# Kernel optimization log

Hardware: AMD Instinct MI355X
Metric: run time of the kernel (lower is better)

Reference implementation:

```python
import jax, jax.numpy as jnp
import numpy as np

N_NODES = 100_000
N_EDGES = 800_000
D_EDGE = 64
D_NODE = 64
D_GLOBAL = 64
D_IN = D_EDGE + 2 * D_NODE + D_GLOBAL  # 256
D_HID = 128
D_OUT = 64


def setup_inputs() -> dict:
    key = jax.random.key(0)
    ks = jax.random.split(key, 8)
    edge_feats = jax.random.normal(ks[0], (N_EDGES, D_EDGE), dtype=jnp.float32)
    node_feats = jax.random.normal(ks[1], (N_NODES, D_NODE), dtype=jnp.float32)
    global_attr = jax.random.normal(ks[2], (D_GLOBAL,), dtype=jnp.float32)
    senders = jax.random.randint(ks[3], (N_EDGES,), 0, N_NODES, dtype=jnp.int32)
    receivers = jax.random.randint(ks[4], (N_EDGES,), 0, N_NODES, dtype=jnp.int32)
    W1 = jax.random.normal(ks[5], (D_IN, D_HID), dtype=jnp.float32) * (1.0 / np.sqrt(D_IN))
    b1 = jnp.zeros((D_HID,), dtype=jnp.float32)
    W2 = jax.random.normal(ks[6], (D_HID, D_OUT), dtype=jnp.float32) * (1.0 / np.sqrt(D_HID))
    b2 = jnp.zeros((D_OUT,), dtype=jnp.float32)
    return {
        "edge_feats": edge_feats,
        "node_feats": node_feats,
        "global_attr": global_attr,
        "senders": senders,
        "receivers": receivers,
        "W1": W1, "b1": b1, "W2": W2, "b2": b2,
    }


def reference(edge_feats, node_feats, global_attr, senders, receivers, W1, b1, W2, b2):
    # Per-edge concat of [edge.data, receiver.data, sender.data, global.data]
    # (torch.cat order in the original), stacked over all edges.
    E = edge_feats.shape[0]
    recv = node_feats[receivers]          # [E, D_NODE] gather
    send = node_feats[senders]            # [E, D_NODE] gather
    g = jnp.broadcast_to(global_attr[None, :], (E, global_attr.shape[0]))
    x = jnp.concatenate([edge_feats, recv, send, g], axis=-1)  # [E, 256]
    # Updater MLP on the stacked edge batch.
    h = jax.nn.relu(x @ W1 + b1)          # [E, 128]
    out = h @ W2 + b2                     # [E, 64]
    return out
```

## Files before the change

kernel.cpp:

```cpp
#include <hip/hip_runtime.h>
#include <hip/hip_bf16.h>


typedef __bf16 bf16x8 __attribute__((ext_vector_type(8)));
typedef __bf16 bf16x2 __attribute__((ext_vector_type(2)));
typedef float f32x4 __attribute__((ext_vector_type(4)));

#define GRID_MAIN 2048
#define WS_NODEBF_OFF 66560

__global__ void prep_kernel(const float* __restrict__ W1, const float* __restrict__ b1,
                            const float* __restrict__ W2, const float* __restrict__ gattr,
                            __bf16* __restrict__ W1F, __bf16* __restrict__ W2F,
                            float* __restrict__ g1) {
    int tid = blockIdx.x * blockDim.x + threadIdx.x;
    if (tid < 128 * 192) {
        int n = tid / 192, k = tid % 192;
        int w = n >> 5, nt2 = (n >> 4) & 1, c = n & 15;
        int f = k >> 5, g = (k >> 3) & 3, j = k & 7;
        W1F[((((w * 2 + nt2) * 6 + f) * 64) + c + 16 * g) * 8 + j] = (__bf16)W1[k * 128 + n];
    } else if (tid < 128 * 192 + 64 * 128) {
        int t = tid - 128 * 192;
        int n = t / 128, p = t % 128;
        int w = n >> 4, c = n & 15;
        int ks = p >> 5, g = (p >> 3) & 3, j = p & 7;
        int klog = (p >> 5) * 32 + (p & 1) * 16 + ((p >> 1) & 15);
        W2F[(((w * 4 + ks) * 64) + c + 16 * g) * 8 + j] = (__bf16)W2[klog * 64 + n];
    } else if (tid < 128 * 192 + 64 * 128 + 128) {
        int n = tid - (128 * 192 + 64 * 128);
        float acc = b1[n];
        for (int j = 0; j < 64; ++j) acc += gattr[j] * W1[(192 + j) * 128 + n];
        g1[n] = acc;
    }
}

__global__ __launch_bounds__(256) void node_conv_kernel(const float* __restrict__ nf,
                                                        __bf16* __restrict__ nb, int n8) {
    int t = blockIdx.x * blockDim.x + threadIdx.x;
    if (t < n8) {
        f32x4 a = *(const f32x4*)(nf + (long)t * 8);
        f32x4 b = *(const f32x4*)(nf + (long)t * 8 + 4);
        bf16x8 o;
#pragma unroll
        for (int j = 0; j < 4; ++j) { o[j] = (__bf16)a[j]; o[4 + j] = (__bf16)b[j]; }
        *(bf16x8*)(nb + (long)t * 8) = o;
    }
}

__device__ __forceinline__ f32x4 mk4(float v) {
    f32x4 r; r[0] = v; r[1] = v; r[2] = v; r[3] = v; return r;
}

__device__ __forceinline__ bf16x8 cvt8(f32x4 lo, f32x4 hi) {
    bf16x8 t;
#pragma unroll
    for (int j = 0; j < 4; ++j) { t[j] = (__bf16)lo[j]; t[4 + j] = (__bf16)hi[j]; }
    return t;
}

__global__ __launch_bounds__(256) void edge_mlp_kernel(
    const float* __restrict__ edge_feats, const __bf16* __restrict__ node_bf,
    const int* __restrict__ senders, const int* __restrict__ receivers,
    const __bf16* __restrict__ W1F, const __bf16* __restrict__ W2F,
    const float* __restrict__ g1, const float* __restrict__ b2,
    float* __restrict__ out, int E, int numTiles)
{
    __shared__ __bf16 A_lds[4 * 6 * 64 * 8];
    __shared__ __bf16 h_frag[4 * 4 * 64 * 8];

    const int lane = threadIdx.x & 63;
    const int w    = threadIdx.x >> 6;
    const int c    = lane & 15;
    const int g    = lane >> 4;
    const int G    = gridDim.x;

    bf16x8 wb1[2][6];
#pragma unroll
    for (int nt2 = 0; nt2 < 2; ++nt2)
#pragma unroll
        for (int f = 0; f < 6; ++f)
            wb1[nt2][f] = *(const bf16x8*)(W1F + (((w * 2 + nt2) * 6 + f) * 64 + lane) * 8);
    bf16x8 wb2[4];
#pragma unroll
    for (int ks = 0; ks < 4; ++ks)
        wb2[ks] = *(const bf16x8*)(W2F + ((w * 4 + ks) * 64 + lane) * 8);
    const float g1v0 = g1[w * 32 + c];
    const float g1v1 = g1[w * 32 + 16 + c];
    const float b2v  = b2[w * 16 + c];

    bf16x8 snr0, snr1, sns0, sns1;
    f32x4 se0, se1, se2, se3;
    int iR, iS;
    {
        long rc = (long)blockIdx.x * 64 + w * 16 + c;
        if (rc > (long)E - 1) rc = (long)E - 1;
        iR = receivers[rc]; iS = senders[rc];
        const __bf16* pr = node_bf + ((long)iR << 6) + g * 8;
        const __bf16* ps = node_bf + ((long)iS << 6) + g * 8;
        snr0 = *(const bf16x8*)(pr);
        snr1 = *(const bf16x8*)(pr + 32);
        sns0 = *(const bf16x8*)(ps);
        sns1 = *(const bf16x8*)(ps + 32);
        const float* pe = edge_feats + (rc << 6) + g * 8;
        se0 = *(const f32x4*)(pe);      se1 = *(const f32x4*)(pe + 4);
        se2 = *(const f32x4*)(pe + 32); se3 = *(const f32x4*)(pe + 36);
        if (blockIdx.x + G < numTiles) {
            long rc2 = (long)(blockIdx.x + G) * 64 + w * 16 + c;
            if (rc2 > (long)E - 1) rc2 = (long)E - 1;
            iR = receivers[rc2]; iS = senders[rc2];
        }
    }

    for (int t = blockIdx.x; t < numTiles; t += G) {
        __bf16* ab = A_lds + w * 6 * 512 + lane * 8;
        *(bf16x8*)(ab)        = cvt8(se0, se1);
        *(bf16x8*)(ab + 512)  = cvt8(se2, se3);
        *(bf16x8*)(ab + 1024) = snr0;
        *(bf16x8*)(ab + 1536) = snr1;
        *(bf16x8*)(ab + 2048) = sns0;
        *(bf16x8*)(ab + 2560) = sns1;

        const int tn = t + G;
        if (tn < numTiles) {
            const __bf16* pr = node_bf + ((long)iR << 6) + g * 8;
            const __bf16* ps = node_bf + ((long)iS << 6) + g * 8;
            snr0 = *(const bf16x8*)(pr);
            snr1 = *(const bf16x8*)(pr + 32);
            sns0 = *(const bf16x8*)(ps);
            sns1 = *(const bf16x8*)(ps + 32);
            long rce = (long)tn * 64 + w * 16 + c;
            if (rce > (long)E - 1) rce = (long)E - 1;
            const float* pe = edge_feats + (rce << 6) + g * 8;
            se0 = *(const f32x4*)(pe);      se1 = *(const f32x4*)(pe + 4);
            se2 = *(const f32x4*)(pe + 32); se3 = *(const f32x4*)(pe + 36);
            if (tn + G < numTiles) {
                long rc2 = (long)(tn + G) * 64 + w * 16 + c;
                if (rc2 > (long)E - 1) rc2 = (long)E - 1;
                iR = receivers[rc2]; iS = senders[rc2];
            }
        }
        __builtin_amdgcn_sched_barrier(0);

        asm volatile("s_waitcnt lgkmcnt(0)" ::: "memory");
        __builtin_amdgcn_s_barrier();

        f32x4 acc0[4], acc1[4];
#pragma unroll
        for (int mt = 0; mt < 4; ++mt) { acc0[mt] = mk4(g1v0); acc1[mt] = mk4(g1v1); }
#pragma unroll
        for (int mt = 0; mt < 4; ++mt)
#pragma unroll
            for (int f = 0; f < 6; ++f) {
                bf16x8 a = *(const bf16x8*)(A_lds + ((mt * 6 + f) * 64 + lane) * 8);
                acc0[mt] = __builtin_amdgcn_mfma_f32_16x16x32_bf16(a, wb1[0][f], acc0[mt], 0, 0, 0);
                acc1[mt] = __builtin_amdgcn_mfma_f32_16x16x32_bf16(a, wb1[1][f], acc1[mt], 0, 0, 0);
            }

#pragma unroll
        for (int mt = 0; mt < 4; ++mt)
#pragma unroll
            for (int r = 0; r < 4; ++r) {
                float v0 = acc0[mt][r]; v0 = v0 > 0.f ? v0 : 0.f;
                float v1 = acc1[mt][r]; v1 = v1 > 0.f ? v1 : 0.f;
                bf16x2 pk; pk[0] = (__bf16)v0; pk[1] = (__bf16)v1;
                *(bf16x2*)&h_frag[(((mt * 4 + w) * 64 + (g * 4 + r) * 4 + (c >> 2)) << 3)
                                  + ((c & 3) << 1)] = pk;
            }

        asm volatile("s_waitcnt lgkmcnt(0)" ::: "memory");
        __builtin_amdgcn_s_barrier();

        f32x4 acc2[4];
#pragma unroll
        for (int mt = 0; mt < 4; ++mt) acc2[mt] = mk4(b2v);
#pragma unroll
        for (int mt = 0; mt < 4; ++mt)
#pragma unroll
            for (int ks = 0; ks < 4; ++ks) {
                bf16x8 ah = *(const bf16x8*)&h_frag[((mt * 4 + ks) * 64 + c * 4 + g) * 8];
                acc2[mt] = __builtin_amdgcn_mfma_f32_16x16x32_bf16(ah, wb2[ks], acc2[mt], 0, 0, 0);
            }

#pragma unroll
        for (int mt = 0; mt < 4; ++mt)
#pragma unroll
            for (int r = 0; r < 4; ++r) {
                long orow = (long)t * 64 + mt * 16 + g * 4 + r;
                if (orow < E) out[orow * 64 + w * 16 + c] = acc2[mt][r];
            }

        asm volatile("s_waitcnt lgkmcnt(0)" ::: "memory");
        __builtin_amdgcn_s_barrier();
    }
}

__global__ __launch_bounds__(256) void edge_mlp_fallback(
    const float* __restrict__ edge_feats, const float* __restrict__ node_feats,
    const int* __restrict__ senders, const int* __restrict__ receivers,
    const __bf16* __restrict__ W1F, const __bf16* __restrict__ W2F,
    const float* __restrict__ g1, const float* __restrict__ b2,
    float* __restrict__ out, int E, int numTiles)
{
    __shared__ __bf16 A_lds[4 * 6 * 64 * 8];
    __shared__ __bf16 h_frag[4 * 4 * 64 * 8];
    const int lane = threadIdx.x & 63;
    const int w = threadIdx.x >> 6;
    const int c = lane & 15;
    const int g = lane >> 4;
    const int G = gridDim.x;

    bf16x8 wb1[2][6];
#pragma unroll
    for (int nt2 = 0; nt2 < 2; ++nt2)
#pragma unroll
        for (int f = 0; f < 6; ++f)
            wb1[nt2][f] = *(const bf16x8*)(W1F + (((w * 2 + nt2) * 6 + f) * 64 + lane) * 8);
    bf16x8 wb2[4];
#pragma unroll
    for (int ks = 0; ks < 4; ++ks)
        wb2[ks] = *(const bf16x8*)(W2F + ((w * 4 + ks) * 64 + lane) * 8);
    const float g1v0 = g1[w * 32 + c];
    const float g1v1 = g1[w * 32 + 16 + c];
    const float b2v  = b2[w * 16 + c];

    for (int t = blockIdx.x; t < numTiles; t += G) {
        long rowc = (long)t * 64 + w * 16 + c;
        if (rowc > (long)E - 1) rowc = (long)E - 1;
        int iR = receivers[rowc], iS = senders[rowc];
        const float* pr = node_feats + ((long)iR << 6) + g * 8;
        const float* ps = node_feats + ((long)iS << 6) + g * 8;
        const float* pe = edge_feats + (rowc << 6) + g * 8;
        f32x4 e0a = *(const f32x4*)(pe),      e0b = *(const f32x4*)(pe + 4);
        f32x4 e1a = *(const f32x4*)(pe + 32), e1b = *(const f32x4*)(pe + 36);
        f32x4 r0a = *(const f32x4*)(pr),      r0b = *(const f32x4*)(pr + 4);
        f32x4 r1a = *(const f32x4*)(pr + 32), r1b = *(const f32x4*)(pr + 36);
        f32x4 s0a = *(const f32x4*)(ps),      s0b = *(const f32x4*)(ps + 4);
        f32x4 s1a = *(const f32x4*)(ps + 32), s1b = *(const f32x4*)(ps + 36);

        __bf16* ab = A_lds + w * 6 * 512 + lane * 8;
        *(bf16x8*)(ab)        = cvt8(e0a, e0b);
        *(bf16x8*)(ab + 512)  = cvt8(e1a, e1b);
        *(bf16x8*)(ab + 1024) = cvt8(r0a, r0b);
        *(bf16x8*)(ab + 1536) = cvt8(r1a, r1b);
        *(bf16x8*)(ab + 2048) = cvt8(s0a, s0b);
        *(bf16x8*)(ab + 2560) = cvt8(s1a, s1b);
        __syncthreads();

        f32x4 acc0[4], acc1[4];
#pragma unroll
        for (int mt = 0; mt < 4; ++mt) { acc0[mt] = mk4(g1v0); acc1[mt] = mk4(g1v1); }
#pragma unroll
        for (int mt = 0; mt < 4; ++mt)
#pragma unroll
            for (int f = 0; f < 6; ++f) {
                bf16x8 a = *(const bf16x8*)(A_lds + ((mt * 6 + f) * 64 + lane) * 8);
                acc0[mt] = __builtin_amdgcn_mfma_f32_16x16x32_bf16(a, wb1[0][f], acc0[mt], 0, 0, 0);
                acc1[mt] = __builtin_amdgcn_mfma_f32_16x16x32_bf16(a, wb1[1][f], acc1[mt], 0, 0, 0);
            }
#pragma unroll
        for (int mt = 0; mt < 4; ++mt)
#pragma unroll
            for (int r = 0; r < 4; ++r) {
                float v0 = acc0[mt][r]; v0 = v0 > 0.f ? v0 : 0.f;
                float v1 = acc1[mt][r]; v1 = v1 > 0.f ? v1 : 0.f;
                bf16x2 pk; pk[0] = (__bf16)v0; pk[1] = (__bf16)v1;
                *(bf16x2*)&h_frag[(((mt * 4 + w) * 64 + (g * 4 + r) * 4 + (c >> 2)) << 3)
                                  + ((c & 3) << 1)] = pk;
            }
        __syncthreads();

        f32x4 acc2[4];
#pragma unroll
        for (int mt = 0; mt < 4; ++mt) acc2[mt] = mk4(b2v);
#pragma unroll
        for (int mt = 0; mt < 4; ++mt)
#pragma unroll
            for (int ks = 0; ks < 4; ++ks) {
                bf16x8 ah = *(const bf16x8*)&h_frag[((mt * 4 + ks) * 64 + c * 4 + g) * 8];
                acc2[mt] = __builtin_amdgcn_mfma_f32_16x16x32_bf16(ah, wb2[ks], acc2[mt], 0, 0, 0);
            }
#pragma unroll
        for (int mt = 0; mt < 4; ++mt)
#pragma unroll
            for (int r = 0; r < 4; ++r) {
                long orow = (long)t * 64 + mt * 16 + g * 4 + r;
                if (orow < E) out[orow * 64 + w * 16 + c] = acc2[mt][r];
            }
        __syncthreads();
    }
}

extern "C" void kernel_launch(void* const* d_in, const int* in_sizes, int n_in,
                              void* d_out, int out_size, void* d_ws, size_t ws_size,
                              hipStream_t stream) {
    const float* edge_feats = (const float*)d_in[0];
    const float* node_feats = (const float*)d_in[1];
    const float* gattr      = (const float*)d_in[2];
    const int*   senders    = (const int*)d_in[3];
    const int*   receivers  = (const int*)d_in[4];
    const float* W1         = (const float*)d_in[5];
    const float* b1         = (const float*)d_in[6];
    const float* W2         = (const float*)d_in[7];
    const float* b2         = (const float*)d_in[8];
    float* out = (float*)d_out;

    const int E = in_sizes[3];
    const int N = in_sizes[1] / 64;

    char* ws = (char*)d_ws;
    __bf16* W1F = (__bf16*)ws;
    __bf16* W2F = (__bf16*)(ws + 49152);
    float*  g1  = (float*)(ws + 49152 + 16384);
    __bf16* nodeBF = (__bf16*)(ws + WS_NODEBF_OFF);

    const size_t ws_needed = (size_t)WS_NODEBF_OFF + (size_t)N * 64 * 2;
    const bool useNB = ws_size >= ws_needed;

    int prep_total = 128 * 192 + 64 * 128 + 128;
    prep_kernel<<<(prep_total + 255) / 256, 256, 0, stream>>>(W1, b1, W2, gattr, W1F, W2F, g1);

    const int numTiles = (E + 63) / 64;
    int grid = numTiles < GRID_MAIN ? numTiles : GRID_MAIN;
    if (useNB) {
        int n8 = N * 8;
        node_conv_kernel<<<(n8 + 255) / 256, 256, 0, stream>>>(node_feats, nodeBF, n8);
        edge_mlp_kernel<<<grid, 256, 0, stream>>>(edge_feats, nodeBF, senders, receivers,
                                                  W1F, W2F, g1, b2, out, E, numTiles);
    } else {
        edge_mlp_fallback<<<grid, 256, 0, stream>>>(edge_feats, node_feats, senders, receivers,
                                                    W1F, W2F, g1, b2, out, E, numTiles);
    }
}
```

Before: 124.0 us.

## Swizzle hidden LDS buffer, prefetch indices two tiles ahead, drop trailing barrier

```diff
diff --git a/kernel.cpp b/kernel.cpp
--- a/kernel.cpp
+++ b/kernel.cpp
@@ -7,6 +7,7 @@
 typedef float f32x4 __attribute__((ext_vector_type(4)));
 
 #define GRID_MAIN 2048
+#define SWZ(x) ((x) ^ (((x) >> 3) & 7))
 #define WS_NODEBF_OFF 66560
 
 __global__ void prep_kernel(const float* __restrict__ W1, const float* __restrict__ b1,
@@ -65,8 +66,7 @@
     const float* __restrict__ g1, const float* __restrict__ b2,
     float* __restrict__ out, int E, int numTiles)
 {
-    __shared__ __bf16 A_lds[4 * 6 * 64 * 8];
-    __shared__ __bf16 h_frag[4 * 4 * 64 * 8];
+    __shared__ __bf16 smem[20480];
 
     const int lane = threadIdx.x & 63;
     const int w    = threadIdx.x >> 6;
@@ -88,31 +88,36 @@
     const float g1v1 = g1[w * 32 + 16 + c];
     const float b2v  = b2[w * 16 + c];
 
+    const int sr = SWZ(c * 4 + g);
+
+    auto rowof = [&](int i) {
+        long r_ = ((long)blockIdx.x + (long)i * G) * 64 + w * 16 + c;
+        return r_ > (long)E - 1 ? (long)E - 1 : r_;
+    };
+
     bf16x8 snr0, snr1, sns0, sns1;
     f32x4 se0, se1, se2, se3;
-    int iR, iS;
+    int iRa, iSa, iRb, iSb;
     {
-        long rc = (long)blockIdx.x * 64 + w * 16 + c;
-        if (rc > (long)E - 1) rc = (long)E - 1;
-        iR = receivers[rc]; iS = senders[rc];
-        const __bf16* pr = node_bf + ((long)iR << 6) + g * 8;
-        const __bf16* ps = node_bf + ((long)iS << 6) + g * 8;
+        long r0 = rowof(0);
+        int iR0 = receivers[r0], iS0 = senders[r0];
+        const __bf16* pr = node_bf + ((long)iR0 << 6) + g * 8;
+        const __bf16* ps = node_bf + ((long)iS0 << 6) + g * 8;
         snr0 = *(const bf16x8*)(pr);
         snr1 = *(const bf16x8*)(pr + 32);
         sns0 = *(const bf16x8*)(ps);
         sns1 = *(const bf16x8*)(ps + 32);
-        const float* pe = edge_feats + (rc << 6) + g * 8;
+        const float* pe = edge_feats + (r0 << 6) + g * 8;
         se0 = *(const f32x4*)(pe);      se1 = *(const f32x4*)(pe + 4);
         se2 = *(const f32x4*)(pe + 32); se3 = *(const f32x4*)(pe + 36);
-        if (blockIdx.x + G < numTiles) {
-            long rc2 = (long)(blockIdx.x + G) * 64 + w * 16 + c;
-            if (rc2 > (long)E - 1) rc2 = (long)E - 1;
-            iR = receivers[rc2]; iS = senders[rc2];
-        }
+        long r1 = rowof(1);
+        iRa = receivers[r1]; iSa = senders[r1];
+        long r2 = rowof(2);
+        iRb = receivers[r2]; iSb = senders[r2];
     }
 
     for (int t = blockIdx.x; t < numTiles; t += G) {
-        __bf16* ab = A_lds + w * 6 * 512 + lane * 8;
+        __bf16* ab = smem + w * 3072 + lane * 8;
         *(bf16x8*)(ab)        = cvt8(se0, se1);
         *(bf16x8*)(ab + 512)  = cvt8(se2, se3);
         *(bf16x8*)(ab + 1024) = snr0;
@@ -120,24 +125,23 @@
         *(bf16x8*)(ab + 2048) = sns0;
         *(bf16x8*)(ab + 2560) = sns1;
 
-        const int tn = t + G;
-        if (tn < numTiles) {
-            const __bf16* pr = node_bf + ((long)iR << 6) + g * 8;
-            const __bf16* ps = node_bf + ((long)iS << 6) + g * 8;
+        {
+            const __bf16* pr = node_bf + ((long)iRa << 6) + g * 8;
+            const __bf16* ps = node_bf + ((long)iSa << 6) + g * 8;
             snr0 = *(const bf16x8*)(pr);
             snr1 = *(const bf16x8*)(pr + 32);
             sns0 = *(const bf16x8*)(ps);
             sns1 = *(const bf16x8*)(ps + 32);
-            long rce = (long)tn * 64 + w * 16 + c;
+            long rce = rowof(1);
+            rce = ((long)t + G) * 64 + w * 16 + c;
             if (rce > (long)E - 1) rce = (long)E - 1;
             const float* pe = edge_feats + (rce << 6) + g * 8;
             se0 = *(const f32x4*)(pe);      se1 = *(const f32x4*)(pe + 4);
             se2 = *(const f32x4*)(pe + 32); se3 = *(const f32x4*)(pe + 36);
-            if (tn + G < numTiles) {
-                long rc2 = (long)(tn + G) * 64 + w * 16 + c;
-                if (rc2 > (long)E - 1) rc2 = (long)E - 1;
-                iR = receivers[rc2]; iS = senders[rc2];
-            }
+            iRa = iRb; iSa = iSb;
+            long r3 = ((long)t + 3L * G) * 64 + w * 16 + c;
+            if (r3 > (long)E - 1) r3 = (long)E - 1;
+            iRb = receivers[r3]; iSb = senders[r3];
         }
         __builtin_amdgcn_sched_barrier(0);
 
@@ -151,7 +155,7 @@
         for (int mt = 0; mt < 4; ++mt)
 #pragma unroll
             for (int f = 0; f < 6; ++f) {
-                bf16x8 a = *(const bf16x8*)(A_lds + ((mt * 6 + f) * 64 + lane) * 8);
+                bf16x8 a = *(const bf16x8*)(smem + ((mt * 6 + f) * 64 + lane) * 8);
                 acc0[mt] = __builtin_amdgcn_mfma_f32_16x16x32_bf16(a, wb1[0][f], acc0[mt], 0, 0, 0);
                 acc1[mt] = __builtin_amdgcn_mfma_f32_16x16x32_bf16(a, wb1[1][f], acc1[mt], 0, 0, 0);
             }
@@ -163,8 +167,9 @@
                 float v0 = acc0[mt][r]; v0 = v0 > 0.f ? v0 : 0.f;
                 float v1 = acc1[mt][r]; v1 = v1 > 0.f ? v1 : 0.f;
                 bf16x2 pk; pk[0] = (__bf16)v0; pk[1] = (__bf16)v1;
-                *(bf16x2*)&h_frag[(((mt * 4 + w) * 64 + (g * 4 + r) * 4 + (c >> 2)) << 3)
-                                  + ((c & 3) << 1)] = pk;
+                int s = g * 16 + r * 4 + (c >> 2);
+                s = SWZ(s);
+                *(bf16x2*)&smem[12288 + (mt * 4 + w) * 512 + s * 8 + ((c & 3) << 1)] = pk;
             }
 
         asm volatile("s_waitcnt lgkmcnt(0)" ::: "memory");
@@ -177,7 +182,7 @@
         for (int mt = 0; mt < 4; ++mt)
 #pragma unroll
             for (int ks = 0; ks < 4; ++ks) {
-                bf16x8 ah = *(const bf16x8*)&h_frag[((mt * 4 + ks) * 64 + c * 4 + g) * 8];
+                bf16x8 ah = *(const bf16x8*)&smem[12288 + (mt * 4 + ks) * 512 + sr * 8];
                 acc2[mt] = __builtin_amdgcn_mfma_f32_16x16x32_bf16(ah, wb2[ks], acc2[mt], 0, 0, 0);
             }
 
@@ -188,9 +193,6 @@
                 long orow = (long)t * 64 + mt * 16 + g * 4 + r;
                 if (orow < E) out[orow * 64 + w * 16 + c] = acc2[mt][r];
             }
-
-        asm volatile("s_waitcnt lgkmcnt(0)" ::: "memory");
-        __builtin_amdgcn_s_barrier();
     }
 }
 
```

New measurement: 127.6 us. 1.03x slower.
